# Optimization experiments

Hardware: AMD Instinct MI355X
Metric: run time of the kernel (lower is better)

The kernel has to match this reference:

```python
import jax, jax.numpy as jnp
import numpy as np

B, M, D = 4, 2048, 1024
N, P = 64, 32  # num_experts, slots_per_expert


def setup_inputs() -> dict:
    key = jax.random.key(0)
    k1, k2, k3, k4 = jax.random.split(key, 4)
    x = jax.random.normal(k1, (B, M, D), dtype=jnp.float32)
    phi = jax.random.normal(k2, (D, N, P), dtype=jnp.float32) * (1.0 / np.sqrt(D))
    W = jax.random.normal(k3, (N, D, D), dtype=jnp.float32) * (1.0 / np.sqrt(D))
    b = jax.random.normal(k4, (N, D), dtype=jnp.float32) * 0.01
    return {"x": x, "phi": phi, "W": W, "b": b}


def reference(x, phi, W, b):
    # logits: (b, m, n, p)
    logits = jnp.einsum('bmd,dnp->bmnp', x, phi)
    # dispatch: softmax over dim=0 (batch), faithful to the given source
    dispatch = jax.nn.softmax(logits, axis=0)
    # combine: softmax over flattened (n*p) slot axis
    bsz, m, n, p = logits.shape
    combine = jax.nn.softmax(logits.reshape(bsz, m, n * p), axis=-1).reshape(bsz, m, n, p)
    # slot inputs: (b, n, p, d)
    slots = jnp.einsum('bmd,bmnp->bnpd', x, dispatch)
    # per-expert GEMM + bias
    y = jnp.einsum('bnpd,nde->bnpe', slots, W) + b[None, :, None, :]
    # combine back to tokens: (b, m, d)
    out = jnp.einsum('bnpd,bmnp->bmd', y, combine)
    return out
```

## Files before the change

kernel.cpp:

```cpp
#include <hip/hip_runtime.h>
#include <hip/hip_bf16.h>
#include <cstddef>

#define Bb 4
#define Mm 2048
#define Dd 1024
#define Nn 64
#define Pp 32
#define NP 2048
#define BM 8192

typedef __attribute__((ext_vector_type(4))) float v4f;
typedef __attribute__((ext_vector_type(8))) short v8s;

__device__ inline unsigned short f2b(float f) {
  union { float f; unsigned u; } v; v.f = f;
  unsigned r = v.u + 0x7fff + ((v.u >> 16) & 1);
  return (unsigned short)(r >> 16);
}

__device__ inline void gld16(const void* g, void* l) {
  __builtin_amdgcn_global_load_lds(
      (const __attribute__((address_space(1))) unsigned*)g,
      (__attribute__((address_space(3))) unsigned*)l, 16, 0, 0);
}

__global__ __launch_bounds__(256) void k_xprep(const float* __restrict__ x,
                                               unsigned short* __restrict__ xb,
                                               unsigned short* __restrict__ xT) {
  __shared__ unsigned short t[32][33];
  const int b = blockIdx.z;
  const int r0 = blockIdx.y * 32;
  const int c0 = blockIdx.x * 32;
  const float* ib = x + (size_t)b * Mm * Dd;
  const int tr = threadIdx.x >> 3;
  const int tc = (threadIdx.x & 7) * 4;
  float4 v = *(const float4*)&ib[(size_t)(r0 + tr) * Dd + c0 + tc];
  ushort4 s;
  s.x = f2b(v.x); s.y = f2b(v.y); s.z = f2b(v.z); s.w = f2b(v.w);
  *(ushort4*)&xb[(size_t)b * Mm * Dd + (size_t)(r0 + tr) * Dd + c0 + tc] = s;
  t[tr][tc + 0] = s.x; t[tr][tc + 1] = s.y;
  t[tr][tc + 2] = s.z; t[tr][tc + 3] = s.w;
  __syncthreads();
  ushort4 o;
  o.x = t[tc + 0][tr]; o.y = t[tc + 1][tr];
  o.z = t[tc + 2][tr]; o.w = t[tc + 3][tr];
  *(ushort4*)&xT[(size_t)b * Dd * Mm + (size_t)(c0 + tr) * Mm + r0 + tc] = o;
}

__global__ __launch_bounds__(256) void k_tr_f2b(const float* __restrict__ in,
                                                unsigned short* __restrict__ out,
                                                int R, int C) {
  __shared__ unsigned short t[32][33];
  const int r0 = blockIdx.y * 32, c0 = blockIdx.x * 32;
  const int tr = threadIdx.x >> 3;
  const int tc = (threadIdx.x & 7) * 4;
  float4 v = *(const float4*)&in[(size_t)(r0 + tr) * C + c0 + tc];
  t[tr][tc + 0] = f2b(v.x); t[tr][tc + 1] = f2b(v.y);
  t[tr][tc + 2] = f2b(v.z); t[tr][tc + 3] = f2b(v.w);
  __syncthreads();
  ushort4 o;
  o.x = t[tc + 0][tr]; o.y = t[tc + 1][tr];
  o.z = t[tc + 2][tr]; o.w = t[tc + 3][tr];
  *(ushort4*)&out[(size_t)(c0 + tr) * R + r0 + tc] = o;
}

__global__ __launch_bounds__(256) void k_tr_b2b(const unsigned short* __restrict__ in, size_t sin_,
                                                unsigned short* __restrict__ out, size_t sout,
                                                int R, int C) {
  __shared__ unsigned short t[32][33];
  const int r0 = blockIdx.y * 32, c0 = blockIdx.x * 32;
  const unsigned short* ib = in + (size_t)blockIdx.z * sin_;
  unsigned short* ob = out + (size_t)blockIdx.z * sout;
  const int tr = threadIdx.x >> 3;
  const int tc = (threadIdx.x & 7) * 4;
  ushort4 v = *(const ushort4*)&ib[(size_t)(r0 + tr) * C + c0 + tc];
  t[tr][tc + 0] = v.x; t[tr][tc + 1] = v.y;
  t[tr][tc + 2] = v.z; t[tr][tc + 3] = v.w;
  __syncthreads();
  ushort4 o;
  o.x = t[tc + 0][tr]; o.y = t[tc + 1][tr];
  o.z = t[tc + 2][tr]; o.w = t[tc + 3][tr];
  *(ushort4*)&ob[(size_t)(c0 + tr) * R + r0 + tc] = o;
}

template <int OUT_BF16>
__global__ __launch_bounds__(256) void k_gemm(const unsigned short* __restrict__ A, size_t sA,
                                              const unsigned short* __restrict__ B, size_t sB,
                                              void* __restrict__ C, size_t sC,
                                              int M, int N, int K) {
  __shared__ unsigned short As[2][128][32];
  __shared__ unsigned short Bs[2][128][32];
  const int tid = threadIdx.x;
  const int wv = tid >> 6, ln = tid & 63;
  const int wm = wv & 1, wn = wv >> 1;
  const int row0 = blockIdx.y * 128, col0 = blockIdx.x * 128;
  const unsigned short* Ab = A + (size_t)blockIdx.z * sA + (size_t)row0 * K;
  const unsigned short* Bbp = B + (size_t)blockIdx.z * sB + (size_t)col0 * K;
  const int sr = ln >> 2;
  const int sc = (ln & 3) * 8;
  const int fr = ln & 15, fc = (ln >> 4) * 8;
  v4f acc[4][4];
#pragma unroll
  for (int i = 0; i < 4; ++i)
#pragma unroll
    for (int j = 0; j < 4; ++j) { v4f z = {0.f, 0.f, 0.f, 0.f}; acc[i][j] = z; }

  for (int kt = 0; kt < K; kt += 64) {
    __syncthreads();
    const size_t ga1 = (size_t)(32 * wv + sr) * K + kt + sc;
    const size_t ga2 = (size_t)(32 * wv + 16 + sr) * K + kt + sc;
    gld16(Ab + ga1,       &As[0][32 * wv][0]);
    gld16(Ab + ga2,       &As[0][32 * wv + 16][0]);
    gld16(Ab + ga1 + 32,  &As[1][32 * wv][0]);
    gld16(Ab + ga2 + 32,  &As[1][32 * wv + 16][0]);
    gld16(Bbp + ga1,      &Bs[0][32 * wv][0]);
    gld16(Bbp + ga2,      &Bs[0][32 * wv + 16][0]);
    gld16(Bbp + ga1 + 32, &Bs[1][32 * wv][0]);
    gld16(Bbp + ga2 + 32, &Bs[1][32 * wv + 16][0]);
    __syncthreads();
#pragma unroll
    for (int ks = 0; ks < 2; ++ks) {
      v8s a[4], b[4];
#pragma unroll
      for (int i = 0; i < 4; ++i) a[i] = *(const v8s*)&As[ks][64 * wm + 16 * i + fr][fc];
#pragma unroll
      for (int j = 0; j < 4; ++j) b[j] = *(const v8s*)&Bs[ks][64 * wn + 16 * j + fr][fc];
#pragma unroll
      for (int i = 0; i < 4; ++i)
#pragma unroll
        for (int j = 0; j < 4; ++j)
          acc[i][j] = __builtin_amdgcn_mfma_f32_16x16x32_bf16(a[i], b[j], acc[i][j], 0, 0, 0);
    }
  }
  const int er = (ln >> 4) * 4, ec = ln & 15;
#pragma unroll
  for (int i = 0; i < 4; ++i)
#pragma unroll
    for (int j = 0; j < 4; ++j) {
      int r = row0 + 64 * wm + 16 * i + er;
      int c = col0 + 64 * wn + 16 * j + ec;
      if (OUT_BF16) {
        unsigned short* Cp = (unsigned short*)C + (size_t)blockIdx.z * sC + (size_t)r * N + c;
#pragma unroll
        for (int q = 0; q < 4; ++q) Cp[(size_t)q * N] = f2b(acc[i][j][q]);
      } else {
        float* Cp = (float*)C + (size_t)blockIdx.z * sC + (size_t)r * N + c;
#pragma unroll
        for (int q = 0; q < 4; ++q) Cp[(size_t)q * N] = acc[i][j][q];
      }
    }
}

__global__ __launch_bounds__(256) void k_softmax(const float* __restrict__ logits,
                                                 unsigned short* __restrict__ dispatch,
                                                 unsigned short* __restrict__ combine) {
  __shared__ float sh[Bb][NP];
  __shared__ float redm[Bb][4];
  __shared__ float reds[Bb][4];
  const int m = blockIdx.x;
  const int tid = threadIdx.x;
  const int wv = tid >> 6, ln = tid & 63;
#pragma unroll
  for (int b = 0; b < Bb; ++b) {
    const float4* src = (const float4*)(logits + ((size_t)b * Mm + m) * NP);
#pragma unroll
    for (int it = 0; it < 2; ++it) ((float4*)sh[b])[tid + it * 256] = src[tid + it * 256];
  }
  __syncthreads();
#pragma unroll
  for (int it = 0; it < 8; ++it) {
    int np = tid + it * 256;
    float v0 = sh[0][np], v1 = sh[1][np], v2 = sh[2][np], v3 = sh[3][np];
    float mx = fmaxf(fmaxf(v0, v1), fmaxf(v2, v3));
    float e0 = __expf(v0 - mx), e1 = __expf(v1 - mx);
    float e2 = __expf(v2 - mx), e3 = __expf(v3 - mx);
    float inv = 1.0f / (e0 + e1 + e2 + e3);
    dispatch[((size_t)0 * Mm + m) * NP + np] = f2b(e0 * inv);
    dispatch[((size_t)1 * Mm + m) * NP + np] = f2b(e1 * inv);
    dispatch[((size_t)2 * Mm + m) * NP + np] = f2b(e2 * inv);
    dispatch[((size_t)3 * Mm + m) * NP + np] = f2b(e3 * inv);
  }
#pragma unroll
  for (int b = 0; b < Bb; ++b) {
    float lmax = -3.0e38f;
#pragma unroll
    for (int it = 0; it < 8; ++it) lmax = fmaxf(lmax, sh[b][tid + it * 256]);
#pragma unroll
    for (int o = 32; o > 0; o >>= 1) lmax = fmaxf(lmax, __shfl_xor(lmax, o, 64));
    if (ln == 0) redm[b][wv] = lmax;
    __syncthreads();
    float mx = fmaxf(fmaxf(redm[b][0], redm[b][1]), fmaxf(redm[b][2], redm[b][3]));
    float lsum = 0.0f;
#pragma unroll
    for (int it = 0; it < 8; ++it) {
      int np = tid + it * 256;
      float e = __expf(sh[b][np] - mx);
      sh[b][np] = e;
      lsum += e;
    }
#pragma unroll
    for (int o = 32; o > 0; o >>= 1) lsum += __shfl_xor(lsum, o, 64);
    if (ln == 0) reds[b][wv] = lsum;
    __syncthreads();
    float inv = 1.0f / (reds[b][0] + reds[b][1] + reds[b][2] + reds[b][3]);
#pragma unroll
    for (int it = 0; it < 8; ++it) {
      int np = tid + it * 256;
      combine[((size_t)b * Mm + m) * NP + np] = f2b(sh[b][np] * inv);
    }
  }
}

__global__ __launch_bounds__(256) void k_y_mfma(const unsigned short* __restrict__ slots,
                                                const float* __restrict__ W,
                                                const float* __restrict__ bias,
                                                unsigned short* __restrict__ y) {
  __shared__ unsigned short As[2][128][32];
  __shared__ unsigned short Bs[2][128][40];
  const int n = blockIdx.z;
  const int col0 = blockIdx.x * 128;
  const int tid = threadIdx.x;
  const int wv = tid >> 6, ln = tid & 63;
  const int wm = wv & 1, wn = wv >> 1;
  const int sr = ln >> 2, sc = (ln & 3) * 8;
  const int fr = ln & 15, fc = (ln >> 4) * 8;
  const float* Wn = W + (size_t)n * Dd * Dd;
  v4f acc[4][4];
#pragma unroll
  for (int i = 0; i < 4; ++i)
#pragma unroll
    for (int j = 0; j < 4; ++j) { v4f z = {0.f, 0.f, 0.f, 0.f}; acc[i][j] = z; }

  for (int kt = 0; kt < Dd; kt += 64) {
    __syncthreads();
    {
      int r1 = 32 * wv + sr;
      int r2 = r1 + 16;
      size_t g1 = ((size_t)(r1 >> 5) * NP + n * Pp + (r1 & 31)) * Dd + kt + sc;
      size_t g2 = ((size_t)(r2 >> 5) * NP + n * Pp + (r2 & 31)) * Dd + kt + sc;
      gld16(slots + g1,      &As[0][32 * wv][0]);
      gld16(slots + g2,      &As[0][32 * wv + 16][0]);
      gld16(slots + g1 + 32, &As[1][32 * wv][0]);
      gld16(slots + g2 + 32, &As[1][32 * wv + 16][0]);
    }
#pragma unroll
    for (int buf = 0; buf < 2; ++buf) {
#pragma unroll
      for (int it = 0; it < 2; ++it) {
        int idx = tid + it * 256;
        int k = ((idx >> 2) & 15) * 2;
        int eseg = ((idx & 3) + ((idx >> 6) << 2)) * 4;
        const float* wp = &Wn[(size_t)(kt + buf * 32 + k) * Dd + col0 + eseg];
        float4 r0 = *(const float4*)wp;
        float4 r1 = *(const float4*)(wp + Dd);
        *(__hip_bfloat162*)&Bs[buf][eseg + 0][k] = __float22bfloat162_rn(float2{r0.x, r1.x});
        *(__hip_bfloat162*)&Bs[buf][eseg + 1][k] = __float22bfloat162_rn(float2{r0.y, r1.y});
        *(__hip_bfloat162*)&Bs[buf][eseg + 2][k] = __float22bfloat162_rn(float2{r0.z, r1.z});
        *(__hip_bfloat162*)&Bs[buf][eseg + 3][k] = __float22bfloat162_rn(float2{r0.w, r1.w});
      }
    }
    __syncthreads();
#pragma unroll
    for (int ks = 0; ks < 2; ++ks) {
      v8s a[4], b[4];
#pragma unroll
      for (int i = 0; i < 4; ++i) a[i] = *(const v8s*)&As[ks][64 * wm + 16 * i + fr][fc];
#pragma unroll
      for (int j = 0; j < 4; ++j) b[j] = *(const v8s*)&Bs[ks][64 * wn + 16 * j + fr][fc];
#pragma unroll
      for (int i = 0; i < 4; ++i)
#pragma unroll
        for (int j = 0; j < 4; ++j)
          acc[i][j] = __builtin_amdgcn_mfma_f32_16x16x32_bf16(a[i], b[j], acc[i][j], 0, 0, 0);
    }
  }
  const int er = (ln >> 4) * 4, ec = ln & 15;
  float bv[4];
#pragma unroll
  for (int j = 0; j < 4; ++j) bv[j] = bias[(size_t)n * Dd + col0 + 64 * wn + 16 * j + ec];
#pragma unroll
  for (int i = 0; i < 4; ++i)
#pragma unroll
    for (int j = 0; j < 4; ++j) {
      int c = col0 + 64 * wn + 16 * j + ec;
#pragma unroll
      for (int q = 0; q < 4; ++q) {
        int r = 64 * wm + 16 * i + er + q;
        size_t row = (size_t)(r >> 5) * NP + n * Pp + (r & 31);
        y[row * Dd + c] = f2b(acc[i][j][q] + bv[j]);
      }
    }
}

extern "C" void kernel_launch(void* const* d_in, const int* in_sizes, int n_in,
                              void* d_out, int out_size, void* d_ws, size_t ws_size,
                              hipStream_t stream) {
  const float* x    = (const float*)d_in[0];
  const float* phi  = (const float*)d_in[1];
  const float* W    = (const float*)d_in[2];
  const float* bias = (const float*)d_in[3];
  float* out = (float*)d_out;
  char* ws = (char*)d_ws;

  float*          logits = (float*)(ws);
  unsigned short* disp_b = (unsigned short*)(ws + 67108864);
  unsigned short* comb_b = (unsigned short*)(ws + 100663296);
  unsigned short* dispT  = (unsigned short*)(ws + 134217728);
  unsigned short* xb     = (unsigned short*)(ws + 167772160);
  unsigned short* xT     = (unsigned short*)(ws + 184549376);
  unsigned short* phiT   = (unsigned short*)(ws + 201326592);
  unsigned short* slots  = (unsigned short*)(ws + 209715200);
  unsigned short* y_b    = (unsigned short*)(ws + 226492416);
  unsigned short* yT     = (unsigned short*)(ws + 243269632);

  k_xprep<<<dim3(32, 64, Bb), 256, 0, stream>>>(x, xb, xT);
  k_tr_f2b<<<dim3(64, 32, 1), 256, 0, stream>>>(phi, phiT, Dd, NP);
  k_gemm<0><<<dim3(16, 64, 1), 256, 0, stream>>>(xb, 0, phiT, 0, logits, 0, BM, NP, Dd);
  k_softmax<<<Mm, 256, 0, stream>>>(logits, disp_b, comb_b);
  k_tr_b2b<<<dim3(64, 64, Bb), 256, 0, stream>>>(disp_b, (size_t)Mm * NP, dispT, (size_t)NP * Mm, Mm, NP);
  k_gemm<1><<<dim3(8, 16, Bb), 256, 0, stream>>>(dispT, (size_t)NP * Mm, xT, (size_t)Dd * Mm,
                                                 slots, (size_t)NP * Dd, NP, Dd, Mm);
  k_y_mfma<<<dim3(8, 1, Nn), 256, 0, stream>>>(slots, W, bias, y_b);
  k_tr_b2b<<<dim3(32, 64, Bb), 256, 0, stream>>>(y_b, (size_t)NP * Dd, yT, (size_t)Dd * NP, NP, Dd);
  k_gemm<0><<<dim3(8, 16, Bb), 256, 0, stream>>>(comb_b, (size_t)Mm * NP, yT, (size_t)Dd * NP,
                                                 out, (size_t)Mm * Dd, Mm, Dd, NP);
}
```

Measured before the change: 610.1 us.

## Replace GEMM with 256x256-tile, 4-stage pipelined, swizzled 8-wave kernel

Replaces the 128x128 double-buffered GEMM with a 256x256 tile, 512-thread kernel. It uses a 4-deep ring of LDS buffers filled by asynchronous global-to-LDS loads, waited on with explicit vmcnt. The kernel raises MFMA wave priority during compute and remaps block IDs in a grouped order for L2 locality. The aim is to hide global load latency and increase data reuse per tile in all three large GEMMs. In exchange it uses more LDS and registers, which lowers occupancy, and the smaller grids (e.g. 128 blocks for the batched GEMMs) may underfill the GPU.

```diff
diff --git a/kernel.cpp b/kernel.cpp
--- a/kernel.cpp
+++ b/kernel.cpp
@@ -85,61 +85,91 @@
 }
 
 template <int OUT_BF16>
-__global__ __launch_bounds__(256) void k_gemm(const unsigned short* __restrict__ A, size_t sA,
-                                              const unsigned short* __restrict__ B, size_t sB,
-                                              void* __restrict__ C, size_t sC,
-                                              int M, int N, int K) {
-  __shared__ unsigned short As[2][128][32];
-  __shared__ unsigned short Bs[2][128][32];
+__global__ __launch_bounds__(512, 2) void k_gemm8(const unsigned short* __restrict__ A, size_t sA,
+                                                  const unsigned short* __restrict__ B, size_t sB,
+                                                  void* __restrict__ C, size_t sC,
+                                                  int M, int N, int K, int nbx) {
+  __shared__ unsigned short As[4][256][32];
+  __shared__ unsigned short Bs[4][256][32];
+  const int nwg = (int)gridDim.x;
+  const int bid = (int)blockIdx.x;
+  const int swz = (bid & 7) * (nwg >> 3) + (bid >> 3);
+  const int bx = swz % nbx, by = swz / nbx;
   const int tid = threadIdx.x;
   const int wv = tid >> 6, ln = tid & 63;
-  const int wm = wv & 1, wn = wv >> 1;
-  const int row0 = blockIdx.y * 128, col0 = blockIdx.x * 128;
+  const int wm = wv >> 2, wn = wv & 3;
+  const int row0 = by * 256, col0 = bx * 256;
   const unsigned short* Ab = A + (size_t)blockIdx.z * sA + (size_t)row0 * K;
   const unsigned short* Bbp = B + (size_t)blockIdx.z * sB + (size_t)col0 * K;
-  const int sr = ln >> 2;
-  const int sc = (ln & 3) * 8;
+  const int srow = wv * 32 + (ln >> 2);
+  const int ssc = (ln & 3) * 8;
   const int fr = ln & 15, fc = (ln >> 4) * 8;
-  v4f acc[4][4];
-#pragma unroll
-  for (int i = 0; i < 4; ++i)
+  const int nt = K >> 5;
+  v4f acc[8][4];
+#pragma unroll
+  for (int i = 0; i < 8; ++i)
 #pragma unroll
     for (int j = 0; j < 4; ++j) { v4f z = {0.f, 0.f, 0.f, 0.f}; acc[i][j] = z; }
 
-  for (int kt = 0; kt < K; kt += 64) {
-    __syncthreads();
-    const size_t ga1 = (size_t)(32 * wv + sr) * K + kt + sc;
-    const size_t ga2 = (size_t)(32 * wv + 16 + sr) * K + kt + sc;
-    gld16(Ab + ga1,       &As[0][32 * wv][0]);
-    gld16(Ab + ga2,       &As[0][32 * wv + 16][0]);
-    gld16(Ab + ga1 + 32,  &As[1][32 * wv][0]);
-    gld16(Ab + ga2 + 32,  &As[1][32 * wv + 16][0]);
-    gld16(Bbp + ga1,      &Bs[0][32 * wv][0]);
-    gld16(Bbp + ga2,      &Bs[0][32 * wv + 16][0]);
-    gld16(Bbp + ga1 + 32, &Bs[1][32 * wv][0]);
-    gld16(Bbp + ga2 + 32, &Bs[1][32 * wv + 16][0]);
-    __syncthreads();
-#pragma unroll
-    for (int ks = 0; ks < 2; ++ks) {
-      v8s a[4], b[4];
-#pragma unroll
-      for (int i = 0; i < 4; ++i) a[i] = *(const v8s*)&As[ks][64 * wm + 16 * i + fr][fc];
-#pragma unroll
-      for (int j = 0; j < 4; ++j) b[j] = *(const v8s*)&Bs[ks][64 * wn + 16 * j + fr][fc];
-#pragma unroll
-      for (int i = 0; i < 4; ++i)
-#pragma unroll
-        for (int j = 0; j < 4; ++j)
-          acc[i][j] = __builtin_amdgcn_mfma_f32_16x16x32_bf16(a[i], b[j], acc[i][j], 0, 0, 0);
-    }
-  }
+#define STAGE8(t, buf) do {                                        \
+    size_t ga1 = (size_t)srow * K + (size_t)(t) * 32 + ssc;        \
+    size_t ga2 = ga1 + (size_t)16 * K;                             \
+    gld16(Ab + ga1,  &As[buf][wv * 32][0]);                        \
+    gld16(Ab + ga2,  &As[buf][wv * 32 + 16][0]);                   \
+    gld16(Bbp + ga1, &Bs[buf][wv * 32][0]);                        \
+    gld16(Bbp + ga2, &Bs[buf][wv * 32 + 16][0]);                   \
+  } while (0)
+
+#define COMP8(buf) do {                                            \
+    v8s a[8], b[4];                                                \
+    _Pragma("unroll")                                              \
+    for (int i = 0; i < 8; ++i)                                    \
+      a[i] = *(const v8s*)&As[buf][wm * 128 + 16 * i + fr][fc];    \
+    _Pragma("unroll")                                              \
+    for (int j = 0; j < 4; ++j)                                    \
+      b[j] = *(const v8s*)&Bs[buf][wn * 64 + 16 * j + fr][fc];     \
+    __builtin_amdgcn_s_setprio(1);                                 \
+    _Pragma("unroll")                                              \
+    for (int i = 0; i < 8; ++i)                                    \
+      _Pragma("unroll")                                            \
+      for (int j = 0; j < 4; ++j)                                  \
+        acc[i][j] = __builtin_amdgcn_mfma_f32_16x16x32_bf16(a[i], b[j], acc[i][j], 0, 0, 0); \
+    __builtin_amdgcn_s_setprio(0);                                 \
+  } while (0)
+
+  STAGE8(0, 0);
+  STAGE8(1, 1);
+  STAGE8(2, 2);
+  asm volatile("s_waitcnt vmcnt(8)" ::: "memory");
+  __builtin_amdgcn_s_barrier();
+  __builtin_amdgcn_sched_barrier(0);
+
+  for (int t = 0; t < nt - 3; ++t) {
+    STAGE8(t + 3, (t + 3) & 3);
+    COMP8(t & 3);
+    asm volatile("s_waitcnt vmcnt(8)" ::: "memory");
+    __builtin_amdgcn_s_barrier();
+    __builtin_amdgcn_sched_barrier(0);
+  }
+  COMP8((nt - 3) & 3);
+  asm volatile("s_waitcnt vmcnt(4)" ::: "memory");
+  __builtin_amdgcn_s_barrier();
+  __builtin_amdgcn_sched_barrier(0);
+  COMP8((nt - 2) & 3);
+  asm volatile("s_waitcnt vmcnt(0)" ::: "memory");
+  __builtin_amdgcn_s_barrier();
+  __builtin_amdgcn_sched_barrier(0);
+  COMP8((nt - 1) & 3);
+#undef STAGE8
+#undef COMP8
+
   const int er = (ln >> 4) * 4, ec = ln & 15;
 #pragma unroll
-  for (int i = 0; i < 4; ++i)
+  for (int i = 0; i < 8; ++i)
 #pragma unroll
     for (int j = 0; j < 4; ++j) {
-      int r = row0 + 64 * wm + 16 * i + er;
-      int c = col0 + 64 * wn + 16 * j + ec;
+      int r = row0 + wm * 128 + 16 * i + er;
+      int c = col0 + wn * 64 + 16 * j + ec;
       if (OUT_BF16) {
         unsigned short* Cp = (unsigned short*)C + (size_t)blockIdx.z * sC + (size_t)r * N + c;
 #pragma unroll
@@ -316,13 +346,13 @@
 
   k_xprep<<<dim3(32, 64, Bb), 256, 0, stream>>>(x, xb, xT);
   k_tr_f2b<<<dim3(64, 32, 1), 256, 0, stream>>>(phi, phiT, Dd, NP);
-  k_gemm<0><<<dim3(16, 64, 1), 256, 0, stream>>>(xb, 0, phiT, 0, logits, 0, BM, NP, Dd);
+  k_gemm8<0><<<dim3(256, 1, 1), 512, 0, stream>>>(xb, 0, phiT, 0, logits, 0, BM, NP, Dd, 8);
   k_softmax<<<Mm, 256, 0, stream>>>(logits, disp_b, comb_b);
   k_tr_b2b<<<dim3(64, 64, Bb), 256, 0, stream>>>(disp_b, (size_t)Mm * NP, dispT, (size_t)NP * Mm, Mm, NP);
-  k_gemm<1><<<dim3(8, 16, Bb), 256, 0, stream>>>(dispT, (size_t)NP * Mm, xT, (size_t)Dd * Mm,
-                                                 slots, (size_t)NP * Dd, NP, Dd, Mm);
+  k_gemm8<1><<<dim3(32, 1, Bb), 512, 0, stream>>>(dispT, (size_t)NP * Mm, xT, (size_t)Dd * Mm,
+                                                  slots, (size_t)NP * Dd, NP, Dd, Mm, 4);
   k_y_mfma<<<dim3(8, 1, Nn), 256, 0, stream>>>(slots, W, bias, y_b);
   k_tr_b2b<<<dim3(32, 64, Bb), 256, 0, stream>>>(y_b, (size_t)NP * Dd, yT, (size_t)Dd * NP, NP, Dd);
-  k_gemm<0><<<dim3(8, 16, Bb), 256, 0, stream>>>(comb_b, (size_t)Mm * NP, yT, (size_t)Dd * NP,
-                                                 out, (size_t)Mm * Dd, Mm, Dd, NP);
-}
+  k_gemm8<0><<<dim3(32, 1, Bb), 512, 0, stream>>>(comb_b, (size_t)Mm * NP, yT, (size_t)Dd * NP,
+                                                  out, (size_t)Mm * Dd, Mm, Dd, NP, 4);
+}
```

After: 681.2 us. 11.6% more time.
